# Kernel tuning notes

Measured on AMD Instinct MI355X. Metric: run time of the kernel, lower is better.

## Reference

```python
import jax, jax.numpy as jnp
import numpy as np

D = 1024
H = 16
EPS = 1e-5


def setup_inputs() -> dict:
    key = jax.random.key(0)
    ks = jax.random.split(key, 6)
    B, T, d = 4, 2048, D
    s = 0.02
    return {
        "x": jax.random.normal(ks[0], (B, T, d), jnp.float32),
        "w_attn": jax.random.normal(ks[1], (d, 3 * d), jnp.float32) * s,
        "w_o": jax.random.normal(ks[2], (d, d), jnp.float32) * s,
        "ln1_g": jnp.ones((d,), jnp.float32),
        "ln1_b": jnp.zeros((d,), jnp.float32),
        "ln2_g": jnp.ones((d,), jnp.float32),
        "ln2_b": jnp.zeros((d,), jnp.float32),
        "w_fc": jax.random.normal(ks[3], (d, 4 * d), jnp.float32) * s,
        "b_fc": jnp.zeros((4 * d,), jnp.float32),
        "w_proj": jax.random.normal(ks[4], (4 * d, d), jnp.float32) * s,
        "b_proj": jnp.zeros((d,), jnp.float32),
    }


def _layernorm(x, g, b):
    mu = jnp.mean(x, axis=-1, keepdims=True)
    var = jnp.mean(jnp.square(x - mu), axis=-1, keepdims=True)
    return (x - mu) * jax.lax.rsqrt(var + EPS) * g + b


def _attention(x, w_attn, w_o):
    B, T, d = x.shape
    hd = d // H
    qkv = x @ w_attn  # [B,T,3d]
    q, k, v = jnp.split(qkv, 3, axis=-1)
    q = q.reshape(B, T, H, hd).transpose(0, 2, 1, 3)  # [B,H,T,hd]
    k = k.reshape(B, T, H, hd).transpose(0, 2, 1, 3)
    v = v.reshape(B, T, H, hd).transpose(0, 2, 1, 3)
    att = jnp.einsum("bhqd,bhkd->bhqk", q, k) * (1.0 / np.sqrt(hd))
    mask = jnp.tril(jnp.ones((T, T), bool))
    att = jnp.where(mask, att, jnp.float32(-jnp.inf))
    att = jax.nn.softmax(att, axis=-1)
    y = jnp.einsum("bhqk,bhkd->bhqd", att, v)
    y = y.transpose(0, 2, 1, 3).reshape(B, T, d)
    return y @ w_o


def reference(x, w_attn, w_o, ln1_g, ln1_b, ln2_g, ln2_b, w_fc, b_fc, w_proj, b_proj):
    x = x + _attention(_layernorm(x, ln1_g, ln1_b), w_attn, w_o)
    h = _layernorm(x, ln2_g, ln2_b)
    h = jax.nn.gelu(h @ w_fc + b_fc, approximate=True)
    return x + h @ w_proj + b_proj
```

## Files before the change

### kernel.cpp

```cpp
#include <hip/hip_runtime.h>
#include <math.h>

#define D_MODEL 1024
#define NHEAD   16
#define HDIM    64
#define SEQ     2048
#define BATCH   4
#define NROWS   (BATCH*SEQ)

using bf16x8 = __attribute__((ext_vector_type(8))) short;
using bf16x4 = __attribute__((ext_vector_type(4))) short;
using f32x4  = __attribute__((ext_vector_type(4))) float;

__device__ __forceinline__ unsigned short f2bf(float f) {
    unsigned u = __float_as_uint(f);
    u += 0x7fffu + ((u >> 16) & 1u);
    return (unsigned short)(u >> 16);
}
__device__ __forceinline__ float bf2f(unsigned short h) {
    unsigned u = ((unsigned)h) << 16;
    return __uint_as_float(u);
}

#define ASYNC_COPY16(g, l) \
    __builtin_amdgcn_global_load_lds((__attribute__((address_space(1))) const void*)(g), \
                                     (__attribute__((address_space(3))) void*)(l), 16, 0, 0)

__global__ __launch_bounds__(256) void ln_kernel(const float* __restrict__ x,
                                                 const float* __restrict__ g,
                                                 const float* __restrict__ b,
                                                 unsigned short* __restrict__ out) {
    const int row = blockIdx.x;
    const int tid = threadIdx.x;
    const float4* x4 = (const float4*)(x + (size_t)row * D_MODEL);
    float4 v = x4[tid];
    float s  = v.x + v.y + v.z + v.w;
    float sq = v.x*v.x + v.y*v.y + v.z*v.z + v.w*v.w;
    #pragma unroll
    for (int off = 32; off >= 1; off >>= 1) {
        s  += __shfl_down(s,  off, 64);
        sq += __shfl_down(sq, off, 64);
    }
    __shared__ float rs[4], rq[4];
    const int wave = tid >> 6;
    if ((tid & 63) == 0) { rs[wave] = s; rq[wave] = sq; }
    __syncthreads();
    const float tot  = rs[0] + rs[1] + rs[2] + rs[3];
    const float totq = rq[0] + rq[1] + rq[2] + rq[3];
    const float mu   = tot * (1.0f / D_MODEL);
    const float var  = totq * (1.0f / D_MODEL) - mu * mu;
    const float rstd = rsqrtf(var + 1e-5f);
    const float4 gv = ((const float4*)g)[tid];
    const float4 bv = ((const float4*)b)[tid];
    unsigned short* o = out + (size_t)row * D_MODEL + tid * 4;
    o[0] = f2bf((v.x - mu) * rstd * gv.x + bv.x);
    o[1] = f2bf((v.y - mu) * rstd * gv.y + bv.y);
    o[2] = f2bf((v.z - mu) * rstd * gv.z + bv.z);
    o[3] = f2bf((v.w - mu) * rstd * gv.w + bv.w);
}

__global__ __launch_bounds__(256) void wt_kernel(const float* __restrict__ w,
                                                 unsigned short* __restrict__ wt,
                                                 int K, int N) {
    __shared__ float tile[32][33];
    const int n0 = blockIdx.x * 32, k0 = blockIdx.y * 32;
    const int tx = threadIdx.x & 31, ty = threadIdx.x >> 5;
    #pragma unroll
    for (int j = 0; j < 4; ++j)
        tile[ty + j * 8][tx] = w[(size_t)(k0 + ty + j * 8) * N + n0 + tx];
    __syncthreads();
    #pragma unroll
    for (int j = 0; j < 4; ++j)
        wt[(size_t)(n0 + ty + j * 8) * K + k0 + tx] = f2bf(tile[tx][ty + j * 8]);
}

template<int MODE>
__global__ __launch_bounds__(512, 2) void gemm8(const unsigned short* __restrict__ A,
                                                const unsigned short* __restrict__ Bt,
                                                const float* __restrict__ bias,
                                                unsigned short* __restrict__ outp,
                                                unsigned short* __restrict__ vt_out,
                                                int M, int N, int K, int Kslice) {
    extern __shared__ __align__(16) char smem[];

    const int tid  = threadIdx.x;
    const int lane = tid & 63;
    const int wave = __builtin_amdgcn_readfirstlane(tid >> 6);
    const int quad = lane >> 4, l16 = lane & 15;
    const int wm = wave >> 2, wn = wave & 3;
    const int m0 = blockIdx.x * 256, n0 = blockIdx.y * 256;

    int kbeg = 0, klen = K;
    if (MODE == 1) {
        kbeg = blockIdx.z * Kslice;
        klen = (blockIdx.z == (int)gridDim.z - 1) ? (K - kbeg) : Kslice;
    }
    const int nt = klen >> 6;

    const int r0  = tid >> 2;
    const int gch = ((tid & 3) ^ (r0 & 3)) * 8;
    const unsigned short* Ag0 = A  + (size_t)(m0 + r0) * K + gch + kbeg;
    const unsigned short* Ag1 = Ag0 + (size_t)128 * K;
    const unsigned short* Bg0 = Bt + (size_t)(n0 + r0) * K + gch + kbeg;
    const unsigned short* Bg1 = Bg0 + (size_t)128 * K;
    char* ldsA = smem + tid * 16;
    char* ldsB = smem + 32768 + tid * 16;

#define STG_A(kh, tt, bb) do { const int ko_ = (tt)*64 + (kh)*32;             \
        ASYNC_COPY16(Ag0 + ko_, ldsA + (bb)*65536 + (kh)*16384);              \
        ASYNC_COPY16(Ag1 + ko_, ldsA + (bb)*65536 + (kh)*16384 + 8192); } while (0)
#define STG_B(kh, tt, bb) do { const int ko_ = (tt)*64 + (kh)*32;             \
        ASYNC_COPY16(Bg0 + ko_, ldsB + (bb)*65536 + (kh)*16384);              \
        ASYNC_COPY16(Bg1 + ko_, ldsB + (bb)*65536 + (kh)*16384 + 8192); } while (0)

    const int coff = (quad ^ (l16 & 3)) * 16;
    const char* rdA = smem + (wm * 128 + l16) * 64 + coff;
    const char* rdB = smem + 32768 + (wn * 64 + l16) * 64 + coff;

    f32x4 acc[8][4] = {};

    STG_A(0, 0, 0); STG_B(0, 0, 0); STG_A(1, 0, 0); STG_B(1, 0, 0);
    STG_A(0, 1, 1); STG_B(0, 1, 1); STG_A(1, 1, 1);
    asm volatile("s_waitcnt vmcnt(6)\n\ts_barrier" ::: "memory");

    for (int t = 0; t < nt; ++t) {
        const int cur = t & 1;
        const char* bA = rdA + cur * 65536;
        const char* bB = rdB + cur * 65536;
        bf16x8 a[8], b0, b1;

        #pragma unroll
        for (int i = 0; i < 8; ++i) a[i] = *(const bf16x8*)(bA + i * 1024);
        b0 = *(const bf16x8*)(bB);
        b1 = *(const bf16x8*)(bB + 1024);
        if (t + 1 < nt) STG_B(1, t + 1, cur ^ 1);
        asm volatile("s_barrier" ::: "memory");
        __builtin_amdgcn_s_setprio(1);
        #pragma unroll
        for (int i = 0; i < 8; ++i) {
            acc[i][0] = __builtin_amdgcn_mfma_f32_16x16x32_bf16(a[i], b0, acc[i][0], 0, 0, 0);
            acc[i][1] = __builtin_amdgcn_mfma_f32_16x16x32_bf16(a[i], b1, acc[i][1], 0, 0, 0);
        }
        __builtin_amdgcn_s_setprio(0);
        asm volatile("s_barrier" ::: "memory");

        b0 = *(const bf16x8*)(bB + 2048);
        b1 = *(const bf16x8*)(bB + 3072);
        if (t + 2 < nt) STG_A(0, t + 2, cur);
        asm volatile("s_barrier" ::: "memory");
        __builtin_amdgcn_s_setprio(1);
        #pragma unroll
        for (int i = 0; i < 8; ++i) {
            acc[i][2] = __builtin_amdgcn_mfma_f32_16x16x32_bf16(a[i], b0, acc[i][2], 0, 0, 0);
            acc[i][3] = __builtin_amdgcn_mfma_f32_16x16x32_bf16(a[i], b1, acc[i][3], 0, 0, 0);
        }
        __builtin_amdgcn_s_setprio(0);
        asm volatile("s_barrier" ::: "memory");

        #pragma unroll
        for (int i = 0; i < 8; ++i) a[i] = *(const bf16x8*)(bA + 16384 + i * 1024);
        b0 = *(const bf16x8*)(bB + 16384);
        b1 = *(const bf16x8*)(bB + 16384 + 1024);
        if (t + 2 < nt) STG_B(0, t + 2, cur);
        asm volatile("s_barrier" ::: "memory");
        __builtin_amdgcn_s_setprio(1);
        #pragma unroll
        for (int i = 0; i < 8; ++i) {
            acc[i][0] = __builtin_amdgcn_mfma_f32_16x16x32_bf16(a[i], b0, acc[i][0], 0, 0, 0);
            acc[i][1] = __builtin_amdgcn_mfma_f32_16x16x32_bf16(a[i], b1, acc[i][1], 0, 0, 0);
        }
        __builtin_amdgcn_s_setprio(0);
        asm volatile("s_barrier" ::: "memory");

        b0 = *(const bf16x8*)(bB + 16384 + 2048);
        b1 = *(const bf16x8*)(bB + 16384 + 3072);
        if (t + 2 < nt) STG_A(1, t + 2, cur);
        asm volatile("s_barrier" ::: "memory");
        __builtin_amdgcn_s_setprio(1);
        #pragma unroll
        for (int i = 0; i < 8; ++i) {
            acc[i][2] = __builtin_amdgcn_mfma_f32_16x16x32_bf16(a[i], b0, acc[i][2], 0, 0, 0);
            acc[i][3] = __builtin_amdgcn_mfma_f32_16x16x32_bf16(a[i], b1, acc[i][3], 0, 0, 0);
        }
        __builtin_amdgcn_s_setprio(0);
        if (t + 2 < nt) asm volatile("s_waitcnt vmcnt(6)\n\ts_barrier" ::: "memory");
        else            asm volatile("s_waitcnt vmcnt(0)\n\ts_barrier" ::: "memory");
    }
#undef STG_A
#undef STG_B

    if (MODE == 0) {
        #pragma unroll
        for (int i = 0; i < 8; ++i)
          #pragma unroll
          for (int j = 0; j < 4; ++j)
            #pragma unroll
            for (int r = 0; r < 4; ++r) {
                const int row = m0 + wm * 128 + i * 16 + quad * 4 + r;
                const int col = n0 + wn * 64 + j * 16 + l16;
                float v = acc[i][j][r] + bias[col];
                const float u = 0.7978845608028654f * (v + 0.044715f * v * v * v);
                const float e = __expf(2.0f * u);
                v = 0.5f * v * (2.0f - 2.0f / (e + 1.0f));
                outp[(size_t)row * N + col] = f2bf(v);
            }
    } else if (MODE == 1) {
        unsigned short* outb = outp + (size_t)blockIdx.z * M * N;
        #pragma unroll
        for (int i = 0; i < 8; ++i)
          #pragma unroll
          for (int j = 0; j < 4; ++j)
            #pragma unroll
            for (int r = 0; r < 4; ++r) {
                const int row = m0 + wm * 128 + i * 16 + quad * 4 + r;
                const int col = n0 + wn * 64 + j * 16 + l16;
                outb[(size_t)row * N + col] = f2bf(acc[i][j][r]);
            }
    } else {
        if (n0 < 2048) {
            const float sc = (n0 < 1024) ? 0.125f : 1.0f;
            #pragma unroll
            for (int i = 0; i < 8; ++i)
              #pragma unroll
              for (int j = 0; j < 4; ++j)
                #pragma unroll
                for (int r = 0; r < 4; ++r) {
                    const int row = m0 + wm * 128 + i * 16 + quad * 4 + r;
                    const int col = n0 + wn * 64 + j * 16 + l16;
                    outp[(size_t)row * 2048 + col] = f2bf(acc[i][j][r] * sc);
                }
        } else {
            #pragma unroll
            for (int i = 0; i < 8; ++i)
              #pragma unroll
              for (int j = 0; j < 4; ++j) {
                    const int dv  = n0 - 2048 + wn * 64 + j * 16 + l16;
                    const int tok = m0 + wm * 128 + i * 16 + quad * 4;
                    ushort4 pk;
                    pk.x = f2bf(acc[i][j][0]); pk.y = f2bf(acc[i][j][1]);
                    pk.z = f2bf(acc[i][j][2]); pk.w = f2bf(acc[i][j][3]);
                    *(ushort4*)(vt_out + (size_t)dv * NROWS + tok) = pk;
                }
        }
    }
}

template<int NP>
__global__ __launch_bounds__(256) void reduce_wo_ln2(const float* __restrict__ x,
                                                     const unsigned short* __restrict__ pw,
                                                     const float* __restrict__ g,
                                                     const float* __restrict__ bb,
                                                     float* __restrict__ out,
                                                     unsigned short* __restrict__ lnout) {
    const int row = blockIdx.x;
    const int tid = threadIdx.x;
    const size_t base = (size_t)row * D_MODEL + tid * 4;
    const size_t stride = (size_t)NROWS * D_MODEL;
    float4 v = *(const float4*)(x + base);
    #pragma unroll
    for (int z = 0; z < NP; ++z) {
        ushort4 a = *(const ushort4*)(pw + z * stride + base);
        v.x += bf2f(a.x); v.y += bf2f(a.y); v.z += bf2f(a.z); v.w += bf2f(a.w);
    }
    *(float4*)(out + base) = v;

    float s  = v.x + v.y + v.z + v.w;
    float sq = v.x*v.x + v.y*v.y + v.z*v.z + v.w*v.w;
    #pragma unroll
    for (int off = 32; off >= 1; off >>= 1) {
        s  += __shfl_down(s,  off, 64);
        sq += __shfl_down(sq, off, 64);
    }
    __shared__ float rs[4], rq[4];
    const int wave = tid >> 6;
    if ((tid & 63) == 0) { rs[wave] = s; rq[wave] = sq; }
    __syncthreads();
    const float tot  = rs[0] + rs[1] + rs[2] + rs[3];
    const float totq = rq[0] + rq[1] + rq[2] + rq[3];
    const float mu   = tot * (1.0f / D_MODEL);
    const float var  = totq * (1.0f / D_MODEL) - mu * mu;
    const float rstd = rsqrtf(var + 1e-5f);
    const float4 gv = ((const float4*)g)[tid];
    const float4 bv = ((const float4*)bb)[tid];
    unsigned short* o = lnout + (size_t)row * D_MODEL + tid * 4;
    o[0] = f2bf((v.x - mu) * rstd * gv.x + bv.x);
    o[1] = f2bf((v.y - mu) * rstd * gv.y + bv.y);
    o[2] = f2bf((v.z - mu) * rstd * gv.z + bv.z);
    o[3] = f2bf((v.w - mu) * rstd * gv.w + bv.w);
}

template<int NP>
__global__ __launch_bounds__(256) void reduce_kernel(float* __restrict__ out,
                                                     const unsigned short* __restrict__ pp,
                                                     const float* __restrict__ bias) {
    const int row = blockIdx.x;
    const int c0 = threadIdx.x * 4;
    const size_t base = (size_t)row * D_MODEL + c0;
    const size_t stride = (size_t)NROWS * D_MODEL;
    float4 o = *(float4*)(out + base);
    const float4 bs = *(const float4*)(bias + c0);
    o.x += bs.x; o.y += bs.y; o.z += bs.z; o.w += bs.w;
    #pragma unroll
    for (int z = 0; z < NP; ++z) {
        ushort4 a = *(const ushort4*)(pp + z * stride + base);
        o.x += bf2f(a.x); o.y += bf2f(a.y); o.z += bf2f(a.z); o.w += bf2f(a.w);
    }
    *(float4*)(out + base) = o;
}

__global__ __launch_bounds__(256) void attn_kernel(const unsigned short* __restrict__ qk,
                                                   const unsigned short* __restrict__ VT,
                                                   unsigned short* __restrict__ y) {
    __shared__ __align__(16) unsigned short Qs[128 * 64];
    __shared__ __align__(16) unsigned short Ks[64 * 64];
    __shared__ __align__(16) unsigned short Vs[80 * 64];
    __shared__ __align__(16) unsigned short Ps[128 * 68];

    const int tid  = threadIdx.x;
    const int lane = tid & 63, w = tid >> 6;
    const int quad = lane >> 4, l16 = lane & 15;
    const int s7   = l16 & 7;
    const int pc0  = (quad ^ s7) * 8;
    const int pc1  = ((quad + 4) ^ s7) * 8;
    const int srow = tid >> 3, sp = tid & 7;

    const int pairidx = blockIdx.x;
    const int bh = blockIdx.y;
    const int b = bh >> 4, h = bh & 15;
    const size_t rowbase = (size_t)b * SEQ;
    const unsigned short* Qbase = qk + h * 64;
    const unsigned short* Kbase = qk + 1024 + h * 64;
    const unsigned short* Vbase = VT + (size_t)(h * 64) * NROWS + b * SEQ;

    #pragma unroll
    for (int e = 0; e < 4; ++e) {
        const int off = tid * 4 + e;
        Vs[4096 + off] = (off < 64) ? (unsigned short)0x3F80 : (unsigned short)0;
    }

    for (int phase = 0; phase < 2; ++phase) {
        const int Q = phase ? pairidx : (15 - pairidx);
        const int nkt = 2 * Q + 2;
        const int qg0 = Q * 128;

        #pragma unroll
        for (int i = 0; i < 4; ++i) {
            const int row = i * 32 + srow;
            const int c = sp ^ (row & 7);
            ASYNC_COPY16(Qbase + (rowbase + qg0 + row) * 2048 + c * 8,
                         (char*)Qs + i * 4096 + tid * 16);
        }
        __syncthreads();

        bf16x8 aq[2][2];
        #pragma unroll
        for (int sub = 0; sub < 2; ++sub) {
            const int qrow = sub * 64 + w * 16 + l16;
            aq[sub][0] = *(const bf16x8*)&Qs[qrow * 64 + pc0];
            aq[sub][1] = *(const bf16x8*)&Qs[qrow * 64 + pc1];
        }

        f32x4 o[2][5] = {};

        for (int kt = 0; kt < nkt; ++kt) {
            #pragma unroll
            for (int i = 0; i < 2; ++i) {
                const int row = i * 32 + srow;
                const int c = sp ^ (row & 7);
                ASYNC_COPY16(Kbase + (rowbase + kt * 64 + row) * 2048 + c * 8,
                             (char*)Ks + i * 4096 + tid * 16);
                ASYNC_COPY16(Vbase + (size_t)row * NROWS + kt * 64 + c * 8,
                             (char*)Vs + i * 4096 + tid * 16);
            }
            __syncthreads();

            bf16x8 bk[4][2];
            #pragma unroll
            for (int cb = 0; cb < 4; ++cb) {
                const int krow = cb * 16 + l16;
                bk[cb][0] = *(const bf16x8*)&Ks[krow * 64 + pc0];
                bk[cb][1] = *(const bf16x8*)&Ks[krow * 64 + pc1];
            }

            #pragma unroll
            for (int sub = 0; sub < 2; ++sub) {
                if (kt > 2 * Q + sub) continue;
                f32x4 s[4] = {};
                #pragma unroll
                for (int cb = 0; cb < 4; ++cb) {
                    s[cb] = __builtin_amdgcn_mfma_f32_16x16x32_bf16(aq[sub][0], bk[cb][0], s[cb], 0, 0, 0);
                    s[cb] = __builtin_amdgcn_mfma_f32_16x16x32_bf16(aq[sub][1], bk[cb][1], s[cb], 0, 0, 0);
                }
                const int prow0 = sub * 64 + w * 16 + quad * 4;
                if (kt == 2 * Q + sub) {
                    const int qg = qg0 + prow0;
                    const int kg = kt * 64 + l16;
                    #pragma unroll
                    for (int cb = 0; cb < 4; ++cb)
                        #pragma unroll
                        for (int r = 0; r < 4; ++r) {
                            const float e = __expf(s[cb][r]);
                            const float pv = (kg + cb * 16 > qg + r) ? 0.0f : e;
                            Ps[(prow0 + r) * 68 + cb * 16 + l16] = f2bf(pv);
                        }
                } else {
                    #pragma unroll
                    for (int cb = 0; cb < 4; ++cb)
                        #pragma unroll
                        for (int r = 0; r < 4; ++r)
                            Ps[(prow0 + r) * 68 + cb * 16 + l16] = f2bf(__expf(s[cb][r]));
                }
            }
            __syncthreads();

            bf16x8 bv[5][2];
            #pragma unroll
            for (int db = 0; db < 5; ++db) {
                const int vrow = db * 16 + l16;
                bv[db][0] = *(const bf16x8*)&Vs[vrow * 64 + pc0];
                bv[db][1] = *(const bf16x8*)&Vs[vrow * 64 + pc1];
            }
            #pragma unroll
            for (int sub = 0; sub < 2; ++sub) {
                if (kt > 2 * Q + sub) continue;
                const unsigned short* pb = &Ps[(sub * 64 + w * 16 + l16) * 68];
                bf16x8 ap0, ap1;
                *(bf16x4*)&ap0       = *(const bf16x4*)(pb + quad * 8);
                *((bf16x4*)&ap0 + 1) = *(const bf16x4*)(pb + quad * 8 + 4);
                *(bf16x4*)&ap1       = *(const bf16x4*)(pb + 32 + quad * 8);
                *((bf16x4*)&ap1 + 1) = *(const bf16x4*)(pb + 32 + quad * 8 + 4);
                #pragma unroll
                for (int db = 0; db < 5; ++db) {
                    o[sub][db] = __builtin_amdgcn_mfma_f32_16x16x32_bf16(ap0, bv[db][0], o[sub][db], 0, 0, 0);
                    o[sub][db] = __builtin_amdgcn_mfma_f32_16x16x32_bf16(ap1, bv[db][1], o[sub][db], 0, 0, 0);
                }
            }
            __syncthreads();
        }

        #pragma unroll
        for (int sub = 0; sub < 2; ++sub)
            #pragma unroll
            for (int r = 0; r < 4; ++r) {
                const float lsum = __shfl(o[sub][4][r], lane & 48);
                const float rinv = 1.0f / lsum;
                const int trow = qg0 + sub * 64 + w * 16 + quad * 4 + r;
                unsigned short* yp = y + (rowbase + trow) * (size_t)D_MODEL + h * 64 + l16;
                #pragma unroll
                for (int db = 0; db < 4; ++db)
                    yp[db * 16] = f2bf(o[sub][db][r] * rinv);
            }
    }
}

extern "C" void kernel_launch(void* const* d_in, const int* in_sizes, int n_in,
                              void* d_out, int out_size, void* d_ws, size_t ws_size,
                              hipStream_t stream) {
    (void)in_sizes; (void)n_in; (void)out_size; (void)ws_size;
    const float* x      = (const float*)d_in[0];
    const float* w_attn = (const float*)d_in[1];
    const float* w_o    = (const float*)d_in[2];
    const float* ln1_g  = (const float*)d_in[3];
    const float* ln1_b  = (const float*)d_in[4];
    const float* ln2_g  = (const float*)d_in[5];
    const float* ln2_b  = (const float*)d_in[6];
    const float* w_fc   = (const float*)d_in[7];
    const float* b_fc   = (const float*)d_in[8];
    const float* w_proj = (const float*)d_in[9];
    const float* b_proj = (const float*)d_in[10];
    float* out = (float*)d_out;

    static bool attr_set = false;
    if (!attr_set) {
        hipFuncSetAttribute(reinterpret_cast<const void*>(&gemm8<0>),
                            hipFuncAttributeMaxDynamicSharedMemorySize, 131072);
        hipFuncSetAttribute(reinterpret_cast<const void*>(&gemm8<1>),
                            hipFuncAttributeMaxDynamicSharedMemorySize, 131072);
        hipFuncSetAttribute(reinterpret_cast<const void*>(&gemm8<2>),
                            hipFuncAttributeMaxDynamicSharedMemorySize, 131072);
        attr_set = true;
    }

    char* ws = (char*)d_ws;
    const size_t MiB = 1048576;
    unsigned short* ln_buf  = (unsigned short*)ws;
    unsigned short* qkbuf   = (unsigned short*)(ws + 16 * MiB);
    unsigned short* VTbuf   = (unsigned short*)(ws + 48 * MiB);
    unsigned short* wt_attn = (unsigned short*)(ws + 64 * MiB);
    unsigned short* hbuf    = (unsigned short*)(ws + 64 * MiB);
    unsigned short* wt_o    = (unsigned short*)(ws + 126 * MiB);
    unsigned short* pw      = (unsigned short*)(ws + 16 * MiB);
    unsigned short* wt_fc   = (unsigned short*)(ws + 48 * MiB);
    unsigned short* wt_proj = (unsigned short*)(ws + 56 * MiB);
    unsigned short* pp      = (unsigned short*)ws;

    wt_kernel<<<dim3(3072 / 32, 1024 / 32), 256, 0, stream>>>(w_attn, wt_attn, 1024, 3072);
    wt_kernel<<<dim3(1024 / 32, 1024 / 32), 256, 0, stream>>>(w_o, wt_o, 1024, 1024);

    ln_kernel<<<NROWS, 256, 0, stream>>>(x, ln1_g, ln1_b, ln_buf);

    gemm8<2><<<dim3(NROWS / 256, 3072 / 256), 512, 131072, stream>>>(
        ln_buf, wt_attn, nullptr, qkbuf, VTbuf, NROWS, 3072, 1024, 0);

    attn_kernel<<<dim3(8, BATCH * NHEAD), 256, 0, stream>>>(qkbuf, VTbuf, ln_buf);

    gemm8<1><<<dim3(NROWS / 256, 1024 / 256, 2), 512, 131072, stream>>>(
        ln_buf, wt_o, nullptr, pw, nullptr, NROWS, 1024, 1024, 512);
    reduce_wo_ln2<2><<<NROWS, 256, 0, stream>>>(x, pw, ln2_g, ln2_b, out, ln_buf);

    wt_kernel<<<dim3(4096 / 32, 1024 / 32), 256, 0, stream>>>(w_fc, wt_fc, 1024, 4096);
    wt_kernel<<<dim3(1024 / 32, 4096 / 32), 256, 0, stream>>>(w_proj, wt_proj, 4096, 1024);

    gemm8<0><<<dim3(NROWS / 256, 4096 / 256), 512, 131072, stream>>>(
        ln_buf, wt_fc, b_fc, hbuf, nullptr, NROWS, 4096, 1024, 0);

    gemm8<1><<<dim3(NROWS / 256, 1024 / 256, 2), 512, 131072, stream>>>(
        hbuf, wt_proj, nullptr, pp, nullptr, NROWS, 1024, 4096, 2048);
    reduce_kernel<2><<<NROWS, 256, 0, stream>>>(out, pp, b_proj);
}
```

Before: 515.7 us.

## Store GEMM tiles as full 128-byte K rows with XOR swizzle and reorder staging

The shared-memory tile layout changes from two K-half planes of 64-byte rows to a single plane of 128-byte rows covering all 64 K values, using an 8-way XOR chunk swizzle. Each wave now stages whole rows, with 8 lanes per row, so global loads are wider and more contiguous. All B fragments for the tile are loaded up front into registers, and the staging order shifts to B-low, B-high, A-low, A-high to match the new buffer reuse points. The risks are higher register pressure from the eight B fragments and changed bank-conflict behaviour on the shared-memory reads.

```diff
diff --git a/kernel.cpp b/kernel.cpp
--- a/kernel.cpp
+++ b/kernel.cpp
@@ -97,97 +97,91 @@
     }
     const int nt = klen >> 6;
 
-    const int r0  = tid >> 2;
-    const int gch = ((tid & 3) ^ (r0 & 3)) * 8;
-    const unsigned short* Ag0 = A  + (size_t)(m0 + r0) * K + gch + kbeg;
-    const unsigned short* Ag1 = Ag0 + (size_t)128 * K;
-    const unsigned short* Bg0 = Bt + (size_t)(n0 + r0) * K + gch + kbeg;
-    const unsigned short* Bg1 = Bg0 + (size_t)128 * K;
-    char* ldsA = smem + tid * 16;
-    char* ldsB = smem + 32768 + tid * 16;
-
-#define STG_A(kh, tt, bb) do { const int ko_ = (tt)*64 + (kh)*32;             \
-        ASYNC_COPY16(Ag0 + ko_, ldsA + (bb)*65536 + (kh)*16384);              \
-        ASYNC_COPY16(Ag1 + ko_, ldsA + (bb)*65536 + (kh)*16384 + 8192); } while (0)
-#define STG_B(kh, tt, bb) do { const int ko_ = (tt)*64 + (kh)*32;             \
-        ASYNC_COPY16(Bg0 + ko_, ldsB + (bb)*65536 + (kh)*16384);              \
-        ASYNC_COPY16(Bg1 + ko_, ldsB + (bb)*65536 + (kh)*16384 + 8192); } while (0)
-
-    const int coff = (quad ^ (l16 & 3)) * 16;
-    const char* rdA = smem + (wm * 128 + l16) * 64 + coff;
-    const char* rdB = smem + 32768 + (wn * 64 + l16) * 64 + coff;
+    const int srow   = wave * 16 + (lane >> 3);
+    const int schunk = ((lane & 7) ^ (lane >> 3)) * 8;
+    const unsigned short* AgLo = A  + (size_t)(m0 + srow) * K + schunk + kbeg;
+    const unsigned short* AgHi = AgLo + (size_t)128 * K;
+    const unsigned short* BgLo = Bt + (size_t)(n0 + srow) * K + schunk + kbeg;
+    const unsigned short* BgHi = BgLo + (size_t)128 * K;
+    char* const ldst = smem + wave * 2048 + lane * 16;
+
+#define STG(src, regOff, bb, ko) do {                                          \
+        ASYNC_COPY16((src) + (ko),                ldst + (bb)*65536 + (regOff));        \
+        ASYNC_COPY16((src) + (ko) + (size_t)8*K,  ldst + (bb)*65536 + (regOff) + 1024); \
+    } while (0)
+
+    const int pc = (quad ^ (l16 & 7)) * 16;
+    const char* rA = smem + (wm * 128 + l16) * 128;
+    const char* rB = smem + 32768 + (wn * 64 + l16) * 128;
 
     f32x4 acc[8][4] = {};
 
-    STG_A(0, 0, 0); STG_B(0, 0, 0); STG_A(1, 0, 0); STG_B(1, 0, 0);
-    STG_A(0, 1, 1); STG_B(0, 1, 1); STG_A(1, 1, 1);
+    STG(BgLo, 32768, 0, 0); STG(BgHi, 49152, 0, 0);
+    STG(AgLo, 0,     0, 0); STG(AgHi, 16384, 0, 0);
+    STG(BgLo, 32768, 1, 64); STG(BgHi, 49152, 1, 64); STG(AgLo, 0, 1, 64);
     asm volatile("s_waitcnt vmcnt(6)\n\ts_barrier" ::: "memory");
 
     for (int t = 0; t < nt; ++t) {
         const int cur = t & 1;
-        const char* bA = rdA + cur * 65536;
-        const char* bB = rdB + cur * 65536;
-        bf16x8 a[8], b0, b1;
-
-        #pragma unroll
-        for (int i = 0; i < 8; ++i) a[i] = *(const bf16x8*)(bA + i * 1024);
-        b0 = *(const bf16x8*)(bB);
-        b1 = *(const bf16x8*)(bB + 1024);
-        if (t + 1 < nt) STG_B(1, t + 1, cur ^ 1);
+        const char* bA = rA + cur * 65536;
+        const char* bB = rB + cur * 65536;
+        bf16x8 a[8], bk[8];
+
+        #pragma unroll
+        for (int i = 0; i < 8; ++i) a[i] = *(const bf16x8*)(bA + i * 2048 + pc);
+        #pragma unroll
+        for (int j = 0; j < 4; ++j) {
+            bk[j]     = *(const bf16x8*)(bB + j * 2048 + pc);
+            bk[4 + j] = *(const bf16x8*)(bB + j * 2048 + (pc ^ 64));
+        }
+        if (t + 1 < nt) STG(AgHi, 16384, cur ^ 1, (t + 1) * 64);
         asm volatile("s_barrier" ::: "memory");
         __builtin_amdgcn_s_setprio(1);
         #pragma unroll
         for (int i = 0; i < 8; ++i) {
-            acc[i][0] = __builtin_amdgcn_mfma_f32_16x16x32_bf16(a[i], b0, acc[i][0], 0, 0, 0);
-            acc[i][1] = __builtin_amdgcn_mfma_f32_16x16x32_bf16(a[i], b1, acc[i][1], 0, 0, 0);
+            acc[i][0] = __builtin_amdgcn_mfma_f32_16x16x32_bf16(a[i], bk[0], acc[i][0], 0, 0, 0);
+            acc[i][1] = __builtin_amdgcn_mfma_f32_16x16x32_bf16(a[i], bk[1], acc[i][1], 0, 0, 0);
         }
         __builtin_amdgcn_s_setprio(0);
         asm volatile("s_barrier" ::: "memory");
 
-        b0 = *(const bf16x8*)(bB + 2048);
-        b1 = *(const bf16x8*)(bB + 3072);
-        if (t + 2 < nt) STG_A(0, t + 2, cur);
+        if (t + 2 < nt) STG(BgLo, 32768, cur, (t + 2) * 64);
         asm volatile("s_barrier" ::: "memory");
         __builtin_amdgcn_s_setprio(1);
         #pragma unroll
         for (int i = 0; i < 8; ++i) {
-            acc[i][2] = __builtin_amdgcn_mfma_f32_16x16x32_bf16(a[i], b0, acc[i][2], 0, 0, 0);
-            acc[i][3] = __builtin_amdgcn_mfma_f32_16x16x32_bf16(a[i], b1, acc[i][3], 0, 0, 0);
+            acc[i][2] = __builtin_amdgcn_mfma_f32_16x16x32_bf16(a[i], bk[2], acc[i][2], 0, 0, 0);
+            acc[i][3] = __builtin_amdgcn_mfma_f32_16x16x32_bf16(a[i], bk[3], acc[i][3], 0, 0, 0);
         }
         __builtin_amdgcn_s_setprio(0);
         asm volatile("s_barrier" ::: "memory");
 
         #pragma unroll
-        for (int i = 0; i < 8; ++i) a[i] = *(const bf16x8*)(bA + 16384 + i * 1024);
-        b0 = *(const bf16x8*)(bB + 16384);
-        b1 = *(const bf16x8*)(bB + 16384 + 1024);
-        if (t + 2 < nt) STG_B(0, t + 2, cur);
+        for (int i = 0; i < 8; ++i) a[i] = *(const bf16x8*)(bA + i * 2048 + (pc ^ 64));
+        if (t + 2 < nt) STG(BgHi, 49152, cur, (t + 2) * 64);
         asm volatile("s_barrier" ::: "memory");
         __builtin_amdgcn_s_setprio(1);
         #pragma unroll
         for (int i = 0; i < 8; ++i) {
-            acc[i][0] = __builtin_amdgcn_mfma_f32_16x16x32_bf16(a[i], b0, acc[i][0], 0, 0, 0);
-            acc[i][1] = __builtin_amdgcn_mfma_f32_16x16x32_bf16(a[i], b1, acc[i][1], 0, 0, 0);
+            acc[i][0] = __builtin_amdgcn_mfma_f32_16x16x32_bf16(a[i], bk[4], acc[i][0], 0, 0, 0);
+            acc[i][1] = __builtin_amdgcn_mfma_f32_16x16x32_bf16(a[i], bk[5], acc[i][1], 0, 0, 0);
         }
         __builtin_amdgcn_s_setprio(0);
         asm volatile("s_barrier" ::: "memory");
 
-        b0 = *(const bf16x8*)(bB + 16384 + 2048);
-        b1 = *(const bf16x8*)(bB + 16384 + 3072);
-        if (t + 2 < nt) STG_A(1, t + 2, cur);
+        if (t + 2 < nt) STG(AgLo, 0, cur, (t + 2) * 64);
         asm volatile("s_barrier" ::: "memory");
         __builtin_amdgcn_s_setprio(1);
         #pragma unroll
         for (int i = 0; i < 8; ++i) {
-            acc[i][2] = __builtin_amdgcn_mfma_f32_16x16x32_bf16(a[i], b0, acc[i][2], 0, 0, 0);
-            acc[i][3] = __builtin_amdgcn_mfma_f32_16x16x32_bf16(a[i], b1, acc[i][3], 0, 0, 0);
+            acc[i][2] = __builtin_amdgcn_mfma_f32_16x16x32_bf16(a[i], bk[6], acc[i][2], 0, 0, 0);
+            acc[i][3] = __builtin_amdgcn_mfma_f32_16x16x32_bf16(a[i], bk[7], acc[i][3], 0, 0, 0);
         }
         __builtin_amdgcn_s_setprio(0);
         if (t + 2 < nt) asm volatile("s_waitcnt vmcnt(6)\n\ts_barrier" ::: "memory");
         else            asm volatile("s_waitcnt vmcnt(0)\n\ts_barrier" ::: "memory");
     }
-#undef STG_A
-#undef STG_B
+#undef STG
 
     if (MODE == 0) {
         #pragma unroll
```

Result: faster. 493.1 us (-4.4%).
